# Performance work log

Measured on AMD Instinct MI355X. Metric: run time of the kernel, lower is better.

Reference implementation:

```python
import jax, jax.numpy as jnp
import numpy as np

# irreps structure: 128 channels x (0e,1o,2e,3o); lm dims 1,3,5,7 -> total 16
L_DIMS = [1, 3, 5, 7]
LM_L = np.repeat(np.arange(4), L_DIMS)                 # l index of each of the 16 lm slots
LM_OFF = np.concatenate([[0], np.cumsum(L_DIMS)])      # [0,1,4,9,16]
AVG_NUM_NEIGHBORS = 16.0
N_NODES, N_EDGES = 8000, 128000


def setup_inputs() -> dict:
    key = jax.random.key(0)
    ks = jax.random.split(key, 13)
    return {
        "node_attrs": jax.random.uniform(ks[0], (N_NODES, 10), jnp.float32),
        "node_feats": jax.random.normal(ks[1], (N_NODES, 128), jnp.float32),
        "edge_attrs": jax.random.normal(ks[2], (N_EDGES, 16), jnp.float32),
        "edge_feats": jax.random.normal(ks[3], (N_EDGES, 8), jnp.float32),
        "edge_index": jax.random.randint(ks[4], (2, N_EDGES), 0, N_NODES, jnp.int32),
        "cutoff": jax.random.uniform(ks[5], (N_EDGES, 1), jnp.float32),
        "W_up": jax.random.normal(ks[6], (128, 128), jnp.float32),
        "W_mlp1": jax.random.normal(ks[7], (8, 64), jnp.float32),
        "W_mlp2": jax.random.normal(ks[8], (64, 64), jnp.float32),
        "W_mlp3": jax.random.normal(ks[9], (64, 64), jnp.float32),
        "W_mlp4": jax.random.normal(ks[10], (64, 512), jnp.float32),
        "W_lin": jax.random.normal(ks[11], (4, 128, 128), jnp.float32),
        "W_skip": jax.random.normal(ks[12], (4, 128, 10, 128), jnp.float32),
    }


def reference(node_attrs, node_feats, edge_attrs, edge_feats, edge_index, cutoff,
              W_up, W_mlp1, W_mlp2, W_mlp3, W_mlp4, W_lin, W_skip):
    N = node_feats.shape[0]
    E = edge_attrs.shape[0]
    # linear_up: 128x0e -> 128x0e (e3nn path norm 1/sqrt(fan_in))
    x = (node_feats @ W_up) * (1.0 / np.sqrt(128.0))                # [N,128]
    # radial MLP (FullyConnectedNet, silu, 1/sqrt(fan_in) per layer)
    h = jax.nn.silu((edge_feats @ W_mlp1) * (1.0 / np.sqrt(8.0)))
    h = jax.nn.silu((h @ W_mlp2) * (1.0 / np.sqrt(64.0)))
    h = jax.nn.silu((h @ W_mlp3) * (1.0 / np.sqrt(64.0)))
    tp_weights = (h @ W_mlp4) * (1.0 / np.sqrt(64.0))               # [E,512]
    tp_weights = tp_weights * cutoff                                # cutoff scaling
    w = tp_weights.reshape(E, 128, 4)                               # [E, channel u, path l]
    sender, receiver = edge_index[0], edge_index[1]
    xs = x[sender]                                                  # gather  [E,128]
    mji = w[:, :, LM_L] * xs[:, :, None] * edge_attrs[:, None, :]   # [E,128,16]
    # scatter_sum into receiver nodes
    message = jax.ops.segment_sum(mji.reshape(E, -1), receiver, num_segments=N)
    message = message.reshape(N, 128, 16)
    # linear irreps_mid -> target (per-l 128->128), then / avg_num_neighbors
    outs = []
    for l in range(4):
        blk = message[:, :, LM_OFF[l]:LM_OFF[l + 1]]
        outs.append(jnp.einsum('num,uw->nwm', blk, W_lin[l]) * (1.0 / np.sqrt(128.0)))
    message = jnp.concatenate(outs, axis=-1) / AVG_NUM_NEIGHBORS    # [N,128,16]
    # skip_tp: FullyConnectedTensorProduct(target x 10x0e -> target)
    norm = 1.0 / np.sqrt(128.0 * 10.0)
    outs = []
    for l in range(4):
        blk = message[:, :, LM_OFF[l]:LM_OFF[l + 1]]
        outs.append(jnp.einsum('num,nv,uvw->nwm', blk, node_attrs, W_skip[l]) * norm)
    # reshape_irreps output: [N, channels=128, lm=16]
    return jnp.concatenate(outs, axis=-1)
```

## Files before the change

### kernel.cpp

```cpp
#include <hip/hip_runtime.h>
#include <hip/hip_bf16.h>

#define N_NODES 8000
#define N_EDGES 128000
#define RS8   0.35355339059327373f
#define RS64  0.125f
#define RS128 0.08838834764831845f
#define C1    0.005524271728019903f
#define NORM  0.02795084971874737f

__device__ __forceinline__ float siluf(float v){ return v / (1.f + __expf(-v)); }
__device__ __forceinline__ unsigned short f2bf(float v){
  unsigned int b = __float_as_uint(v);
  b += 0x7fffu + ((b >> 16) & 1u);
  return (unsigned short)(b >> 16);
}
__device__ __forceinline__ float bf2f(unsigned int h){
  union{unsigned int u; float f;} z; z.u = h << 16; return z.f;
}
__device__ __forceinline__ float lo2f(unsigned int p){
  union{unsigned int u; float f;} z; z.u = p << 16; return z.f;
}
__device__ __forceinline__ float hi2f(unsigned int p){
  union{unsigned int u; float f;} z; z.u = p & 0xffff0000u; return z.f;
}

#define WT_U_STRIDE_U4 384

__global__ void __launch_bounds__(256) k_up(const float* __restrict__ nf,
                                            const float* __restrict__ Wup,
                                            float* __restrict__ x){
  __shared__ float f[2][128];
  const int t = threadIdx.x;
  const int nl = t >> 7, c = t & 127;
  const int n = blockIdx.x * 2 + nl;
  f[nl][c] = nf[(size_t)n * 128 + c];
  __syncthreads();
  float acc = 0.f;
  #pragma unroll 8
  for(int k = 0; k < 128; ++k) acc += f[nl][k] * Wup[k * 128 + c];
  x[(size_t)n * 128 + c] = acc * RS128;
}

__device__ __forceinline__ void gemm64(const float* __restrict__ hin, const float* __restrict__ Wb,
                                       int eb, int cb, float4 acc[4]){
  #pragma unroll
  for(int i = 0; i < 4; ++i) acc[i] = make_float4(0.f,0.f,0.f,0.f);
  #pragma unroll 2
  for(int k = 0; k < 64; k += 4){
    float4 w0 = *(const float4*)&Wb[(k+0)*64 + cb];
    float4 w1 = *(const float4*)&Wb[(k+1)*64 + cb];
    float4 w2 = *(const float4*)&Wb[(k+2)*64 + cb];
    float4 w3 = *(const float4*)&Wb[(k+3)*64 + cb];
    #pragma unroll
    for(int i = 0; i < 4; ++i){
      float4 h = *(const float4*)&hin[(eb+i)*64 + k];
      acc[i].x += h.x*w0.x + h.y*w1.x + h.z*w2.x + h.w*w3.x;
      acc[i].y += h.x*w0.y + h.y*w1.y + h.z*w2.y + h.w*w3.y;
      acc[i].z += h.x*w0.z + h.y*w1.z + h.z*w2.z + h.w*w3.z;
      acc[i].w += h.x*w0.w + h.y*w1.w + h.z*w2.w + h.w*w3.w;
    }
  }
}

__global__ void __launch_bounds__(256) k_mlp(
    const float* __restrict__ efg, const float* __restrict__ cut,
    const float* __restrict__ W1g, const float* __restrict__ W2g,
    const float* __restrict__ W3g, const float* __restrict__ W4g,
    __hip_bfloat16* __restrict__ tpw){
  __shared__ float ef[512];
  __shared__ float W1s[512];
  __shared__ float hA[4096];
  __shared__ float hB[4096];
  __shared__ float Wb[4096];
  __shared__ float co[64];
  const int t = threadIdx.x;
  const int e0 = blockIdx.x * 64;
  ((float2*)ef)[t]  = ((const float2*)(efg + (size_t)e0 * 8))[t];
  ((float2*)W1s)[t] = ((const float2*)W1g)[t];
  if(t < 64) co[t] = cut[e0 + t];
  __syncthreads();
  const int et = t >> 4, ct = t & 15;
  const int eb = et * 4, cb = ct * 4;
  {
    float4 acc[4];
    #pragma unroll
    for(int i = 0; i < 4; ++i) acc[i] = make_float4(0.f,0.f,0.f,0.f);
    #pragma unroll
    for(int k = 0; k < 8; ++k){
      float4 wv = *(const float4*)&W1s[k*64 + cb];
      #pragma unroll
      for(int i = 0; i < 4; ++i){
        float h = ef[(eb+i)*8 + k];
        acc[i].x += h*wv.x; acc[i].y += h*wv.y; acc[i].z += h*wv.z; acc[i].w += h*wv.w;
      }
    }
    #pragma unroll
    for(int i = 0; i < 4; ++i){
      float4 r;
      r.x = siluf(acc[i].x*RS8); r.y = siluf(acc[i].y*RS8);
      r.z = siluf(acc[i].z*RS8); r.w = siluf(acc[i].w*RS8);
      *(float4*)&hA[(eb+i)*64 + cb] = r;
    }
  }
  __syncthreads();
  #pragma unroll
  for(int r = 0; r < 8; ++r) ((float2*)Wb)[t + 256*r] = ((const float2*)W2g)[t + 256*r];
  __syncthreads();
  {
    float4 a[4]; gemm64(hA, Wb, eb, cb, a);
    #pragma unroll
    for(int i = 0; i < 4; ++i){
      float4 r;
      r.x = siluf(a[i].x*RS64); r.y = siluf(a[i].y*RS64);
      r.z = siluf(a[i].z*RS64); r.w = siluf(a[i].w*RS64);
      *(float4*)&hB[(eb+i)*64 + cb] = r;
    }
  }
  __syncthreads();
  #pragma unroll
  for(int r = 0; r < 8; ++r) ((float2*)Wb)[t + 256*r] = ((const float2*)W3g)[t + 256*r];
  __syncthreads();
  {
    float4 a[4]; gemm64(hB, Wb, eb, cb, a);
    #pragma unroll
    for(int i = 0; i < 4; ++i){
      float4 r;
      r.x = siluf(a[i].x*RS64); r.y = siluf(a[i].y*RS64);
      r.z = siluf(a[i].z*RS64); r.w = siluf(a[i].w*RS64);
      *(float4*)&hA[(eb+i)*64 + cb] = r;
    }
  }
  __syncthreads();
  for(int ch = 0; ch < 8; ++ch){
    #pragma unroll
    for(int r = 0; r < 16; ++r){
      int idx = t + 256*r;
      Wb[idx] = W4g[(idx >> 6) * 512 + ch * 64 + (idx & 63)];
    }
    __syncthreads();
    float4 a[4]; gemm64(hA, Wb, eb, cb, a);
    #pragma unroll
    for(int i = 0; i < 4; ++i){
      float cf = co[eb + i] * RS64;
      ushort4 pk;
      pk.x = f2bf(a[i].x * cf); pk.y = f2bf(a[i].y * cf);
      pk.z = f2bf(a[i].z * cf); pk.w = f2bf(a[i].w * cf);
      *(ushort4*)((unsigned short*)tpw + (size_t)(e0 + eb + i) * 512 + ch * 64 + cb) = pk;
    }
    __syncthreads();
  }
}

__global__ void k_wm(const float* __restrict__ Wlin, float* __restrict__ Wm){
  int idx = blockIdx.x * 256 + threadIdx.x;
  if(idx >= 16 * 16384) return;
  int m = idx >> 14;
  int l = (m == 0) ? 0 : (m < 4) ? 1 : (m < 9) ? 2 : 3;
  Wm[idx] = Wlin[l * 16384 + (idx & 16383)] * C1;
}

__global__ void __launch_bounds__(256) k_wcvt(const float* __restrict__ Ws,
                                              unsigned short* __restrict__ Wt){
  int tid = blockIdx.x * 256 + threadIdx.x;
  int lg = tid >> 14, u = (tid >> 7) & 127, w = tid & 127;
  unsigned short buf[24];
  #pragma unroll
  for(int p = 0; p < 2; ++p){
    int l = (lg == 0) ? (p == 0 ? 0 : 3) : (p == 0 ? 1 : 2);
    #pragma unroll
    for(int v = 0; v < 10; ++v)
      buf[p * 12 + v] = f2bf(Ws[((size_t)(l * 128 + u) * 10 + v) * 128 + w]);
    buf[p * 12 + 10] = 0; buf[p * 12 + 11] = 0;
  }
  uint4* dst = (uint4*)(Wt + (size_t)tid * 24);
  dst[0] = *(const uint4*)&buf[0];
  dst[1] = *(const uint4*)&buf[8];
  dst[2] = *(const uint4*)&buf[16];
}

__global__ void k_count(const int* __restrict__ recv, int* __restrict__ cnt){
  int e = blockIdx.x * 256 + threadIdx.x;
  if(e < N_EDGES) atomicAdd(&cnt[recv[e]], 1);
}
__global__ void __launch_bounds__(1024) k_scan(const int* __restrict__ cnt, int* __restrict__ off){
  __shared__ int s[1024];
  int t = threadIdx.x;
  int base = t * 8;
  int loc[8]; int sum = 0;
  #pragma unroll
  for(int i = 0; i < 8; ++i){
    int idx = base + i;
    int v = (idx < N_NODES) ? cnt[idx] : 0;
    loc[i] = sum; sum += v;
  }
  s[t] = sum;
  __syncthreads();
  for(int d = 1; d < 1024; d <<= 1){
    int v = (t >= d) ? s[t - d] : 0;
    __syncthreads();
    s[t] += v;
    __syncthreads();
  }
  int excl = (t > 0) ? s[t - 1] : 0;
  #pragma unroll
  for(int i = 0; i < 8; ++i){
    int idx = base + i;
    if(idx <= N_NODES) off[idx] = excl + loc[i];
  }
}
__global__ void k_fill(const int* __restrict__ recv, const int* __restrict__ off,
                       int* __restrict__ cur, int* __restrict__ elist){
  int e = blockIdx.x * 256 + threadIdx.x;
  if(e < N_EDGES){
    int r = recv[e];
    int p = atomicAdd(&cur[r], 1);
    elist[off[r] + p] = e;
  }
}

__global__ void __launch_bounds__(256) k_gather(
    const __hip_bfloat16* __restrict__ tpw, const float* __restrict__ x,
    const float* __restrict__ ea, const int* __restrict__ send,
    const int* __restrict__ off, const int* __restrict__ elist,
    float* __restrict__ msg1){
  const int n = blockIdx.x, t = threadIdx.x;
  const int s0 = off[n], deg = off[n + 1] - s0;
  __shared__ unsigned int wr[256];
  __shared__ float xs[128];
  __shared__ float eas[16];
  float acc[8] = {0.f,0.f,0.f,0.f,0.f,0.f,0.f,0.f};
  const int u = t & 127, mg = t >> 7;
  for(int i = 0; i < deg; ++i){
    int e = elist[s0 + i];
    int snd = send[e];
    __syncthreads();
    wr[t] = ((const unsigned int*)tpw)[(size_t)e * 256 + t];
    if(t < 128) xs[t] = x[(size_t)snd * 128 + t];
    else if(t < 144) eas[t - 128] = ea[(size_t)e * 16 + (t - 128)];
    __syncthreads();
    float xu = xs[u];
    unsigned int p0 = wr[u * 2], p1 = wr[u * 2 + 1];
    float w0 = bf2f(p0 & 0xffffu), w1 = bf2f(p0 >> 16);
    float w2 = bf2f(p1 & 0xffffu), w3 = bf2f(p1 >> 16);
    if(mg == 0){
      acc[0] += w0 * (xu * eas[0]);
      acc[1] += w1 * (xu * eas[1]);
      acc[2] += w1 * (xu * eas[2]);
      acc[3] += w1 * (xu * eas[3]);
      acc[4] += w2 * (xu * eas[4]);
      acc[5] += w2 * (xu * eas[5]);
      acc[6] += w2 * (xu * eas[6]);
      acc[7] += w2 * (xu * eas[7]);
    } else {
      acc[0] += w2 * (xu * eas[8]);
      acc[1] += w3 * (xu * eas[9]);
      acc[2] += w3 * (xu * eas[10]);
      acc[3] += w3 * (xu * eas[11]);
      acc[4] += w3 * (xu * eas[12]);
      acc[5] += w3 * (xu * eas[13]);
      acc[6] += w3 * (xu * eas[14]);
      acc[7] += w3 * (xu * eas[15]);
    }
  }
  float4* dst = (float4*)&msg1[(size_t)n * 2048 + u * 16 + mg * 8];
  dst[0] = make_float4(acc[0], acc[1], acc[2], acc[3]);
  dst[1] = make_float4(acc[4], acc[5], acc[6], acc[7]);
}

__global__ void __launch_bounds__(256) k_lin(const float* __restrict__ msg1,
                                             const float* __restrict__ Wm,
                                             float* __restrict__ msg2){
  const int nb = blockIdx.x * 8;
  __shared__ float m1[8 * 2048];
  const int t = threadIdx.x;
  #pragma unroll
  for(int r = 0; r < 16; ++r){
    int i4 = t + 256 * r;
    ((float4*)m1)[i4] = ((const float4*)(msg1 + (size_t)nb * 2048))[i4];
  }
  __syncthreads();
  const int m = t & 15, g = t >> 4;
  float acc[8][8];
  #pragma unroll
  for(int a = 0; a < 8; ++a)
    #pragma unroll
    for(int b = 0; b < 8; ++b) acc[a][b] = 0.f;
  const float* Wp = Wm + m * 16384 + g * 8;
  for(int k = 0; k < 128; ++k){
    float4 wa = *(const float4*)(Wp + k * 128);
    float4 wb = *(const float4*)(Wp + k * 128 + 4);
    #pragma unroll
    for(int nl = 0; nl < 8; ++nl){
      float mv = m1[nl * 2048 + k * 16 + m];
      acc[nl][0] += mv * wa.x; acc[nl][1] += mv * wa.y;
      acc[nl][2] += mv * wa.z; acc[nl][3] += mv * wa.w;
      acc[nl][4] += mv * wb.x; acc[nl][5] += mv * wb.y;
      acc[nl][6] += mv * wb.z; acc[nl][7] += mv * wb.w;
    }
  }
  #pragma unroll
  for(int nl = 0; nl < 8; ++nl)
    #pragma unroll
    for(int j = 0; j < 8; ++j)
      msg2[(size_t)(nb + nl) * 2048 + (g * 8 + j) * 16 + m] = acc[nl][j];
}

__global__ void __launch_bounds__(512) k_skip(const float* __restrict__ msg2,
                                              const float* __restrict__ attrs,
                                              const unsigned short* __restrict__ Wt,
                                              float* __restrict__ outp){
  const int nb = blockIdx.x * 8;
  const int t = threadIdx.x;
  const int w = t & 127;
  const int ng = t >> 7;
  const int ngrp = ng & 1;
  const int lg = ng >> 1;
  const int n0 = nb + ngrp * 4;

  float av[4][10];
  #pragma unroll
  for(int j = 0; j < 4; ++j)
    #pragma unroll
    for(int v = 0; v < 10; ++v)
      av[j][v] = attrs[(size_t)(n0 + j) * 10 + v];

  const float* m2p = msg2 + (size_t)n0 * 2048;
  const uint4* Wp = (const uint4*)(Wt + ((size_t)(lg * 128) * 128 + w) * 24);

  float acc[4][8];
  #pragma unroll
  for(int j = 0; j < 4; ++j)
    #pragma unroll
    for(int m = 0; m < 8; ++m) acc[j][m] = 0.f;

  #pragma unroll 2
  for(int u = 0; u < 128; ++u){
    uint4 a0 = Wp[(size_t)u * WT_U_STRIDE_U4 + 0];
    uint4 a1 = Wp[(size_t)u * WT_U_STRIDE_U4 + 1];
    uint4 a2 = Wp[(size_t)u * WT_U_STRIDE_U4 + 2];
    float wa0 = lo2f(a0.x), wa1 = hi2f(a0.x), wa2 = lo2f(a0.y), wa3 = hi2f(a0.y);
    float wa4 = lo2f(a0.z), wa5 = hi2f(a0.z), wa6 = lo2f(a0.w), wa7 = hi2f(a0.w);
    float wa8 = lo2f(a1.x), wa9 = hi2f(a1.x);
    float wb0 = lo2f(a1.z), wb1 = hi2f(a1.z), wb2 = lo2f(a1.w), wb3 = hi2f(a1.w);
    float wb4 = lo2f(a2.x), wb5 = hi2f(a2.x), wb6 = lo2f(a2.y), wb7 = hi2f(a2.y);
    float wb8 = lo2f(a2.z), wb9 = hi2f(a2.z);

    float sa[4], sb[4];
    #pragma unroll
    for(int j = 0; j < 4; ++j){
      float s = av[j][0]*wa0 + av[j][1]*wa1 + av[j][2]*wa2 + av[j][3]*wa3 + av[j][4]*wa4
              + av[j][5]*wa5 + av[j][6]*wa6 + av[j][7]*wa7 + av[j][8]*wa8 + av[j][9]*wa9;
      sa[j] = s;
      float r = av[j][0]*wb0 + av[j][1]*wb1 + av[j][2]*wb2 + av[j][3]*wb3 + av[j][4]*wb4
              + av[j][5]*wb5 + av[j][6]*wb6 + av[j][7]*wb7 + av[j][8]*wb8 + av[j][9]*wb9;
      sb[j] = r;
    }

    if(lg == 0){
      #pragma unroll
      for(int j = 0; j < 4; ++j){
        const float* q = m2p + (size_t)j * 2048 + u * 16;
        float  q00 = q[0];
        float4 q2 = *(const float4*)(q + 8);
        float4 q3 = *(const float4*)(q + 12);
        acc[j][0] += q00  * sa[j];
        acc[j][1] += q2.y * sb[j];
        acc[j][2] += q2.z * sb[j];
        acc[j][3] += q2.w * sb[j];
        acc[j][4] += q3.x * sb[j];
        acc[j][5] += q3.y * sb[j];
        acc[j][6] += q3.z * sb[j];
        acc[j][7] += q3.w * sb[j];
      }
    } else {
      #pragma unroll
      for(int j = 0; j < 4; ++j){
        const float* q = m2p + (size_t)j * 2048 + u * 16;
        float4 q0 = *(const float4*)q;
        float4 q1 = *(const float4*)(q + 4);
        float  q8 = q[8];
        acc[j][0] += q0.y * sa[j];
        acc[j][1] += q0.z * sa[j];
        acc[j][2] += q0.w * sa[j];
        acc[j][3] += q1.x * sb[j];
        acc[j][4] += q1.y * sb[j];
        acc[j][5] += q1.z * sb[j];
        acc[j][6] += q1.w * sb[j];
        acc[j][7] += q8   * sb[j];
      }
    }
  }

  if(lg == 0){
    #pragma unroll
    for(int j = 0; j < 4; ++j){
      float* dst = &outp[(size_t)(n0 + j) * 2048 + w * 16];
      dst[0] = acc[j][0] * NORM;
      dst[9] = acc[j][1] * NORM;
      float2 p2; p2.x = acc[j][2] * NORM; p2.y = acc[j][3] * NORM;
      *(float2*)(dst + 10) = p2;
      float4 p4;
      p4.x = acc[j][4] * NORM; p4.y = acc[j][5] * NORM;
      p4.z = acc[j][6] * NORM; p4.w = acc[j][7] * NORM;
      *(float4*)(dst + 12) = p4;
    }
  } else {
    #pragma unroll
    for(int j = 0; j < 4; ++j){
      float* dst = &outp[(size_t)(n0 + j) * 2048 + w * 16];
      dst[1] = acc[j][0] * NORM;
      float2 p2; p2.x = acc[j][1] * NORM; p2.y = acc[j][2] * NORM;
      *(float2*)(dst + 2) = p2;
      float4 p4;
      p4.x = acc[j][3] * NORM; p4.y = acc[j][4] * NORM;
      p4.z = acc[j][5] * NORM; p4.w = acc[j][6] * NORM;
      *(float4*)(dst + 4) = p4;
      dst[8] = acc[j][7] * NORM;
    }
  }
}

extern "C" void kernel_launch(void* const* d_in, const int* in_sizes, int n_in,
                              void* d_out, int out_size, void* d_ws, size_t ws_size,
                              hipStream_t stream){
  const float* node_attrs = (const float*)d_in[0];
  const float* node_feats = (const float*)d_in[1];
  const float* edge_attrs = (const float*)d_in[2];
  const float* edge_feats = (const float*)d_in[3];
  const int*   edge_index = (const int*)d_in[4];
  const float* cutoff     = (const float*)d_in[5];
  const float* W_up  = (const float*)d_in[6];
  const float* W1    = (const float*)d_in[7];
  const float* W2    = (const float*)d_in[8];
  const float* W3    = (const float*)d_in[9];
  const float* W4    = (const float*)d_in[10];
  const float* Wlin  = (const float*)d_in[11];
  const float* Wskip = (const float*)d_in[12];
  float* out = (float*)d_out;

  char* ws = (char*)d_ws;
  float*            x     = (float*)(ws + 0);
  __hip_bfloat16*   tpw   = (__hip_bfloat16*)(ws + 4096000);
  float*            msg2  = (float*)(ws + 4096000);
  float*            msg1  = (float*)(ws + 135168000);
  unsigned short*   Wt16  = (unsigned short*)(ws + 135168000);
  float*            Wm    = (float*)(ws + 200704000);
  int*              cnt   = (int*)(ws + 201752576);
  int*              cur   = (int*)(ws + 201784576);
  int*              offs  = (int*)(ws + 201816576);
  int*              elist = (int*)(ws + 201848640);

  hipMemsetAsync(cnt, 0, 64000, stream);

  k_up    <<<4000, 256, 0, stream>>>(node_feats, W_up, x);
  k_mlp   <<<2000, 256, 0, stream>>>(edge_feats, cutoff, W1, W2, W3, W4, tpw);
  k_wm    <<<1024, 256, 0, stream>>>(Wlin, Wm);
  k_count <<<500,  256, 0, stream>>>(edge_index + N_EDGES, cnt);
  k_scan  <<<1,   1024, 0, stream>>>(cnt, offs);
  k_fill  <<<500,  256, 0, stream>>>(edge_index + N_EDGES, offs, cur, elist);
  k_gather<<<8000, 256, 0, stream>>>(tpw, x, edge_attrs, edge_index, offs, elist, msg1);
  k_lin   <<<1000, 256, 0, stream>>>(msg1, Wm, msg2);
  k_wcvt  <<<128,  256, 0, stream>>>(Wskip, Wt16);
  k_skip  <<<1000, 512, 0, stream>>>(msg2, node_attrs, Wt16, out);
}
```

Measured before the change: 1.056 ms.

## Drop LDS staging in gather, prefetch edge indices, stage msg2 tile in LDS for skip

The gather kernel no longer stages per-edge weights, sender features and edge attributes through shared memory with two barriers per edge. Each thread now loads its own bf16 weight pair, sender feature and edge-attribute float4s directly, and the next edge index and sender are prefetched one iteration ahead. The skip kernel copies the 8-node msg2 tile into 64KB of LDS before its main loop and declares launch bounds requesting 4 blocks. The aim is to remove the barrier stalls and the serialized index chain in the gather, and to cut repeated global reads in the skip. In exchange, global traffic becomes redundant across threads, and the skip kernel's large LDS footprint may limit occupancy below what the launch bounds request.

```diff
diff --git a/kernel.cpp b/kernel.cpp
--- a/kernel.cpp
+++ b/kernel.cpp
@@ -226,41 +226,26 @@
     float* __restrict__ msg1){
   const int n = blockIdx.x, t = threadIdx.x;
   const int s0 = off[n], deg = off[n + 1] - s0;
-  __shared__ unsigned int wr[256];
-  __shared__ float xs[128];
-  __shared__ float eas[16];
+  const int u = t & 127, mg = t >> 7;
   float acc[8] = {0.f,0.f,0.f,0.f,0.f,0.f,0.f,0.f};
-  const int u = t & 127, mg = t >> 7;
+  int e_nxt = 0, s_nxt = 0;
+  if(deg > 0){ e_nxt = elist[s0]; s_nxt = send[e_nxt]; }
   for(int i = 0; i < deg; ++i){
-    int e = elist[s0 + i];
-    int snd = send[e];
-    __syncthreads();
-    wr[t] = ((const unsigned int*)tpw)[(size_t)e * 256 + t];
-    if(t < 128) xs[t] = x[(size_t)snd * 128 + t];
-    else if(t < 144) eas[t - 128] = ea[(size_t)e * 16 + (t - 128)];
-    __syncthreads();
-    float xu = xs[u];
-    unsigned int p0 = wr[u * 2], p1 = wr[u * 2 + 1];
-    float w0 = bf2f(p0 & 0xffffu), w1 = bf2f(p0 >> 16);
-    float w2 = bf2f(p1 & 0xffffu), w3 = bf2f(p1 >> 16);
+    const int e = e_nxt, snd = s_nxt;
+    if(i + 1 < deg){ e_nxt = elist[s0 + i + 1]; s_nxt = send[e_nxt]; }
+    uint2 wp  = *(const uint2*)((const unsigned short*)tpw + (size_t)e * 512 + u * 4);
+    float xu  = x[(size_t)snd * 128 + u];
+    float4 e0 = *(const float4*)(ea + (size_t)e * 16 + mg * 8);
+    float4 e1 = *(const float4*)(ea + (size_t)e * 16 + mg * 8 + 4);
+    float w0 = lo2f(wp.x), w1 = hi2f(wp.x), w2 = lo2f(wp.y), w3 = hi2f(wp.y);
     if(mg == 0){
-      acc[0] += w0 * (xu * eas[0]);
-      acc[1] += w1 * (xu * eas[1]);
-      acc[2] += w1 * (xu * eas[2]);
-      acc[3] += w1 * (xu * eas[3]);
-      acc[4] += w2 * (xu * eas[4]);
-      acc[5] += w2 * (xu * eas[5]);
-      acc[6] += w2 * (xu * eas[6]);
-      acc[7] += w2 * (xu * eas[7]);
+      float a = w0 * xu, b = w1 * xu, c = w2 * xu;
+      acc[0] += a * e0.x; acc[1] += b * e0.y; acc[2] += b * e0.z; acc[3] += b * e0.w;
+      acc[4] += c * e1.x; acc[5] += c * e1.y; acc[6] += c * e1.z; acc[7] += c * e1.w;
     } else {
-      acc[0] += w2 * (xu * eas[8]);
-      acc[1] += w3 * (xu * eas[9]);
-      acc[2] += w3 * (xu * eas[10]);
-      acc[3] += w3 * (xu * eas[11]);
-      acc[4] += w3 * (xu * eas[12]);
-      acc[5] += w3 * (xu * eas[13]);
-      acc[6] += w3 * (xu * eas[14]);
-      acc[7] += w3 * (xu * eas[15]);
+      float c = w2 * xu, d = w3 * xu;
+      acc[0] += c * e0.x; acc[1] += d * e0.y; acc[2] += d * e0.z; acc[3] += d * e0.w;
+      acc[4] += d * e1.x; acc[5] += d * e1.y; acc[6] += d * e1.z; acc[7] += d * e1.w;
     }
   }
   float4* dst = (float4*)&msg1[(size_t)n * 2048 + u * 16 + mg * 8];
@@ -306,12 +291,19 @@
       msg2[(size_t)(nb + nl) * 2048 + (g * 8 + j) * 16 + m] = acc[nl][j];
 }
 
-__global__ void __launch_bounds__(512) k_skip(const float* __restrict__ msg2,
-                                              const float* __restrict__ attrs,
-                                              const unsigned short* __restrict__ Wt,
-                                              float* __restrict__ outp){
+__global__ void __launch_bounds__(512, 4) k_skip(const float* __restrict__ msg2,
+                                                 const float* __restrict__ attrs,
+                                                 const unsigned short* __restrict__ Wt,
+                                                 float* __restrict__ outp){
   const int nb = blockIdx.x * 8;
   const int t = threadIdx.x;
+  __shared__ float m2s[8 * 2048];
+  {
+    const float4* src = (const float4*)(msg2 + (size_t)nb * 2048);
+    float4* dstl = (float4*)m2s;
+    #pragma unroll
+    for(int r = 0; r < 8; ++r) dstl[t + 512 * r] = src[t + 512 * r];
+  }
   const int w = t & 127;
   const int ng = t >> 7;
   const int ngrp = ng & 1;
@@ -325,7 +317,8 @@
     for(int v = 0; v < 10; ++v)
       av[j][v] = attrs[(size_t)(n0 + j) * 10 + v];
 
-  const float* m2p = msg2 + (size_t)n0 * 2048;
+  __syncthreads();
+  const float* m2p = m2s + (ngrp * 4) * 2048;
   const uint4* Wp = (const uint4*)(Wt + ((size_t)(lg * 128) * 128 + w) * 24);
 
   float acc[4][8];
```

Measured after the change: 3.681 ms. +248.5%, slower.
